# Optimization experiments

Hardware: AMD Instinct MI355X
Metric: run time of the kernel (lower is better)

The kernel has to match this reference:

```python
import jax, jax.numpy as jnp
from jax import lax
import numpy as np
from math import lgamma

N_MELS = 80; MEMORY_DIM = 512; PRENET = (256, 256)
ATTN_LSTM = 1024; ATTN_DIM = 128
N_STATIC = 8; SF = 21; N_DYN = 8; DF = 21
PRIOR_LEN = 11; ALPHA = 0.1; BETA = 0.9
DEC_LSTM = 1024; R = 2
B = 32; T_MELS = 800; T_ENC = 200


def _betabinom_pmf(k, n, a, b):
    lbeta = lambda x, y: lgamma(x) + lgamma(y) - lgamma(x + y)
    return np.exp(lgamma(n + 1) - lgamma(k + 1) - lgamma(n - k + 1) + lbeta(k + a, n - k + b) - lbeta(a, b))


def setup_inputs() -> dict:
    key = jax.random.key(0)
    ks = iter(jax.random.split(key, 40))
    w = lambda shape, s=0.05: jax.random.normal(next(ks), shape, jnp.float32) * s
    # prior filter, flipped as in the torch buffer (so cross-correlation == convolution with pmf)
    prior = np.array([_betabinom_pmf(k, PRIOR_LEN - 1, ALPHA, BETA) for k in range(PRIOR_LEN)], np.float32)[::-1].copy()
    return {
        "mels": w((B, N_MELS, T_MELS), 1.0),
        "memory": w((B, T_ENC, MEMORY_DIM), 1.0),
        "prenet_W1": w((PRENET[0], N_MELS)), "prenet_b1": jnp.zeros((PRENET[0],), jnp.float32),
        "prenet_W2": w((PRENET[1], PRENET[0])), "prenet_b2": jnp.zeros((PRENET[1],), jnp.float32),
        "attn_Wih": w((4 * ATTN_LSTM, PRENET[1] + MEMORY_DIM)), "attn_Whh": w((4 * ATTN_LSTM, ATTN_LSTM)),
        "attn_bih": jnp.zeros((4 * ATTN_LSTM,), jnp.float32), "attn_bhh": jnp.zeros((4 * ATTN_LSTM,), jnp.float32),
        "dca_Wq": w((ATTN_DIM, ATTN_LSTM)), "dca_bq": jnp.zeros((ATTN_DIM,), jnp.float32),
        "dca_V": w((N_DYN * DF, ATTN_DIM)),
        "dca_F": w((N_STATIC, 1, SF)),
        "dca_U": w((ATTN_DIM, N_STATIC)),
        "dca_T": w((ATTN_DIM, N_DYN)), "dca_Tb": jnp.zeros((ATTN_DIM,), jnp.float32),
        "dca_v": w((1, ATTN_DIM)),
        "prior": jnp.asarray(prior),
        "dec_Wih": w((4 * DEC_LSTM, ATTN_LSTM + MEMORY_DIM)), "dec_Whh": w((4 * DEC_LSTM, DEC_LSTM)),
        "dec_bih": jnp.zeros((4 * DEC_LSTM,), jnp.float32), "dec_bhh": jnp.zeros((4 * DEC_LSTM,), jnp.float32),
        "ac_W": w((N_MELS * R, DEC_LSTM + MEMORY_DIM)), "ac_b": jnp.zeros((N_MELS * R,), jnp.float32),
    }


def _lstm_cell(x, h, c, Wih, Whh, bih, bhh):
    g = x @ Wih.T + bih + h @ Whh.T + bhh
    i, f, gg, o = jnp.split(g, 4, axis=-1)  # torch gate order i,f,g,o
    c_new = jax.nn.sigmoid(f) * c + jax.nn.sigmoid(i) * jnp.tanh(gg)
    h_new = jax.nn.sigmoid(o) * jnp.tanh(c_new)
    return h_new, c_new


def _conv1d(x, k, pad, groups=1):
    # x: [B, Cin, T], k: [Cout, Cin/groups, K]; cross-correlation, like torch conv1d
    return lax.conv_general_dilated(x, k, (1,), [pad], feature_group_count=groups)


def _dca_step(query, memory, aw, prior, Wq, bq, V, Fk, U, Tw, Tb, v):
    Bsz, T = aw.shape
    # location prior: causal conv with (flipped) betabinom pmf
    p = _conv1d(aw[:, None, :], prior[None, None, :], (PRIOR_LEN - 1, 0))[:, 0, :]
    p = jnp.log(jnp.maximum(p, 1e-6))
    # dynamic filters predicted from query, applied per-batch via grouped conv
    G = jnp.tanh(query @ Wq.T + bq) @ V.T  # [B, N_DYN*DF]
    g = _conv1d(aw[None, :, :], G.reshape(Bsz * N_DYN, 1, DF), ((DF - 1) // 2, (DF - 1) // 2), groups=Bsz)
    g = g.reshape(Bsz, N_DYN, T).transpose(0, 2, 1)  # [B, T, N_DYN]
    # static location filters
    f = _conv1d(aw[:, None, :], Fk, ((SF - 1) // 2, (SF - 1) // 2)).transpose(0, 2, 1)  # [B, T, N_STATIC]
    e = (jnp.tanh(f @ U.T + g @ Tw.T + Tb) @ v.T)[:, :, 0] + p  # [B, T]
    aw_new = jax.nn.softmax(e, axis=-1)
    ctx = jnp.einsum("bt,btd->bd", aw_new, memory)
    return aw_new, ctx


def reference(mels, memory, prenet_W1, prenet_b1, prenet_W2, prenet_b2, attn_Wih, attn_Whh, attn_bih, attn_bhh, dca_Wq, dca_bq, dca_V, dca_F, dca_U, dca_T, dca_Tb, dca_v, prior, dec_Wih, dec_Whh, dec_bih, dec_bhh, ac_W, ac_b):
    Bsz, n_mels, T_mels = mels.shape
    T_enc = memory.shape[1]
    n_steps = T_mels // R
    go = jnp.zeros((Bsz, n_mels), mels.dtype)
    # teacher forcing: step t>0 consumes ground-truth frame at index t*R - 1
    tf = mels[:, :, R - 1::R][:, :, : n_steps - 1].transpose(2, 0, 1)
    frames = jnp.concatenate([go[None], tf], axis=0)  # [S, B, n_mels]
    aw0 = jnp.zeros((Bsz, T_enc), mels.dtype).at[:, 0].set(1.0)  # one-hot init attention
    carry0 = (jnp.zeros((Bsz, MEMORY_DIM), mels.dtype),
              jnp.zeros((Bsz, ATTN_LSTM), mels.dtype), jnp.zeros((Bsz, ATTN_LSTM), mels.dtype),
              jnp.zeros((Bsz, DEC_LSTM), mels.dtype), jnp.zeros((Bsz, DEC_LSTM), mels.dtype),
              aw0)

    def step(carry, frame):
        ctx, ah, acs, dh, dcs, aw = carry
        x = jax.nn.relu(frame @ prenet_W1.T + prenet_b1)
        x = jax.nn.relu(x @ prenet_W2.T + prenet_b2)
        ah, acs = _lstm_cell(jnp.concatenate([ctx, x], -1), ah, acs, attn_Wih, attn_Whh, attn_bih, attn_bhh)
        aw, ctx = _dca_step(ah, memory, aw, prior, dca_Wq, dca_bq, dca_V, dca_F, dca_U, dca_T, dca_Tb, dca_v)
        dh, dcs = _lstm_cell(jnp.concatenate([ah, ctx], -1), dh, dcs, dec_Wih, dec_Whh, dec_bih, dec_bhh)
        out = jnp.concatenate([dh, ctx], -1) @ ac_W.T + ac_b  # [B, n_mels*R]
        return (ctx, ah, acs, dh, dcs, aw), (out, aw)

    _, (outs, aws) = lax.scan(step, carry0, frames)
    # per-step [B, n_mels, R] frames concatenated along time (step-major)
    output_mels = outs.reshape(n_steps, Bsz, n_mels, R).transpose(1, 2, 0, 3).reshape(Bsz, n_mels, n_steps * R)
    alignments = aws.transpose(1, 2, 0)  # [B, T_enc, n_steps]
    return output_mels, alignments
```

## Files before the change

### kernel.cpp

```cpp
#include <hip/hip_runtime.h>
#include <hip/hip_bf16.h>

typedef unsigned short u16;
typedef unsigned int   u32;

#define NTHR 256

#define BATCH 32
#define TENC  200
#define NMELS 80
#define TMELS 800
#define NSTEP 400

#define OFF_AH    0
#define OFF_ACS   65536
#define OFF_DH    98304
#define OFF_DCS   131072
#define OFF_CTX   163840
#define OFF_AW    180224
#define OFF_FBUF  186624
#define OFF_PBUF  237824
#define OFF_GPART 244224
#define OFF_X     375296
#define FLOAT_END 3652096
#define ZERO_CNT  180224

#define B_AWIH 0
#define B_AWHH 3145728
#define B_DWIH 7340032
#define B_DWHH 13631488
#define B_ACW  17825792
#define B_WQ   18071552
#define B_MEMT 18202624

struct KArgs {
  const float *mels, *memory, *pW1, *pb1, *pW2, *pb2;
  const float *aWih, *aWhh, *abih, *abhh;
  const float *Wq, *bq, *V, *F, *U, *T, *Tb, *vv, *prior;
  const float *dWih, *dWhh, *dbih, *dbhh, *acW, *acb;
  float *out;
  float *ws;
  u16   *wb;
};

__device__ __forceinline__ float sigf(float x) {
  x = fminf(fmaxf(x, -30.f), 30.f);
  return 1.0f / (1.0f + __expf(-x));
}
__device__ __forceinline__ float ftanh(float x) {
  x = fminf(fmaxf(x, -15.f), 15.f);
  float e = __expf(2.f * x);
  return (e - 1.f) / (e + 1.f);
}
__device__ __forceinline__ float blo(u32 u) {
  union { u32 i; float f; } v; v.i = u << 16; return v.f;
}
__device__ __forceinline__ float bhi(u32 u) {
  union { u32 i; float f; } v; v.i = u & 0xffff0000u; return v.f;
}
__device__ __forceinline__ u16 f2b(float x) {
  __hip_bfloat16 h = __float2bfloat16(x);
  return *reinterpret_cast<u16*>(&h);
}

__device__ __forceinline__ void loadx(const float* src, float* xin) {
  const float4* p = (const float4*)src;
  #pragma unroll
  for (int q = 0; q < 8; ++q) {
    float4 v = p[q];
    xin[q*4+0] = v.x; xin[q*4+1] = v.y; xin[q*4+2] = v.z; xin[q*4+3] = v.w;
  }
}

__device__ __forceinline__ float dot32b(const float* xin, const u16* w) {
  const uint4* wp = (const uint4*)w;
  float acc = 0.f;
  #pragma unroll
  for (int q = 0; q < 4; ++q) {
    uint4 wv = wp[q];
    acc += blo(wv.x)*xin[q*8+0] + bhi(wv.x)*xin[q*8+1]
         + blo(wv.y)*xin[q*8+2] + bhi(wv.y)*xin[q*8+3]
         + blo(wv.z)*xin[q*8+4] + bhi(wv.z)*xin[q*8+5]
         + blo(wv.w)*xin[q*8+6] + bhi(wv.w)*xin[q*8+7];
  }
  return acc;
}

__device__ __forceinline__ float reduce8(float* smred, const float* acc) {
  const int t = threadIdx.x;
  const int b = t & 31, seg = t >> 5;
  __syncthreads();
  #pragma unroll
  for (int r = 0; r < 8; ++r) smred[(seg*8 + r)*32 + b] = acc[r];
  __syncthreads();
  const int r2 = t >> 5, b2 = t & 31;
  float tot = 0.f;
  #pragma unroll
  for (int sgi = 0; sgi < 8; ++sgi) tot += smred[(sgi*8 + r2)*32 + b2];
  return tot;
}

__device__ __forceinline__ void outproj(const KArgs& a, float* smred,
                                        const float* dh, const float* ctx,
                                        int pb, int sprev) {
  const int tid = threadIdx.x;
  const int b = tid & 31, seg = tid >> 5;
  const u16* wb = a.wb;
  float acc[8];
  #pragma unroll
  for (int r = 0; r < 8; ++r) acc[r] = 0.f;
  #pragma unroll 2
  for (int kc = 0; kc < 6; ++kc) {
    const float* src = (kc < 4) ? (dh + b*1024 + kc*256) : (ctx + b*512 + (kc-4)*256);
    float xin[32];
    loadx(src + seg*32, xin);
    #pragma unroll
    for (int r = 0; r < 8; ++r) {
      const int rr = pb*8 + r;
      acc[r] += dot32b(xin, wb + B_ACW + rr*1536 + kc*256 + seg*32);
    }
  }
  float tot = reduce8(smred, acc);
  const int r2 = tid >> 5, b2 = tid & 31;
  const int rr = pb*8 + r2;
  tot += a.acb[rr];
  a.out[(b2*NMELS + (rr >> 1))*TMELS + sprev*2 + (rr & 1)] = tot;
}

__global__ __launch_bounds__(NTHR) void init_kernel(KArgs a) {
  const int gtid = blockIdx.x*NTHR + threadIdx.x;
  const int str = gridDim.x*NTHR;
  float* ws = a.ws;
  for (int i = gtid; i < ZERO_CNT; i += str) ws[i] = 0.f;
  float* aw = ws + OFF_AW;
  for (int i = gtid; i < BATCH*TENC; i += str) aw[i] = ((i % TENC) == 0) ? 1.f : 0.f;
}

__global__ __launch_bounds__(NTHR) void conv_kernel(KArgs a) {
  const int gtid = blockIdx.x*NTHR + threadIdx.x;
  const int str = gridDim.x*NTHR;
  u16* wb = a.wb;
  for (int i = gtid; i < 3145728; i += str) wb[B_AWIH + i] = f2b(a.aWih[i]);
  for (int i = gtid; i < 4194304; i += str) wb[B_AWHH + i] = f2b(a.aWhh[i]);
  for (int i = gtid; i < 6291456; i += str) wb[B_DWIH + i] = f2b(a.dWih[i]);
  for (int i = gtid; i < 4194304; i += str) wb[B_DWHH + i] = f2b(a.dWhh[i]);
  for (int i = gtid; i < 245760;  i += str) wb[B_ACW  + i] = f2b(a.acW[i]);
  for (int i = gtid; i < 131072;  i += str) wb[B_WQ   + i] = f2b(a.Wq[i]);
  for (int i = gtid; i < 3276800; i += str) {
    const int b = i / 102400, rem = i - b*102400;
    const int d = rem / 200, t = rem - d*200;
    wb[B_MEMT + i] = f2b(a.memory[b*102400 + t*512 + d]);
  }
}

__global__ __launch_bounds__(NTHR) void prenet_kernel(KArgs a) {
  __shared__ float sm[384];
  const int tid = threadIdx.x;
  const int pair = blockIdx.x;
  const int s = pair >> 5, b = pair & 31;
  float* X = a.ws + OFF_X;
  if (tid < 80) {
    float v = 0.f;
    if (s > 0) v = a.mels[(b*NMELS + tid)*TMELS + 2*s - 1];
    sm[tid] = v;
  }
  __syncthreads();
  float a1 = a.pb1[tid];
  #pragma unroll 4
  for (int k = 0; k < 80; ++k) a1 += a.pW1[tid*80 + k] * sm[k];
  a1 = fmaxf(a1, 0.f);
  __syncthreads();
  sm[128 + tid] = a1;
  __syncthreads();
  float a2 = a.pb2[tid];
  #pragma unroll 4
  for (int k = 0; k < 256; ++k) a2 += a.pW2[tid*256 + k] * sm[128 + k];
  a2 = fmaxf(a2, 0.f);
  X[(s*BATCH + b)*256 + tid] = a2;
}

__device__ __forceinline__ void dca_step(const KArgs& a, float* sm, int b, int s,
                                         const float* ah_new, float* aw,
                                         const float* fbuf, const float* pbuf, float* ctx) {
  const int tid = threadIdx.x;
  const u16* wb = a.wb;
  float* s_ah  = sm;
  float* s_awp = sm + 1024;
  float* s_q   = sm + 1248;
  float* s_G   = sm + 1376;
  float* s_e   = sm + 1552;
  float* s_gg  = sm + 1760;
  float* s_ff  = sm + 3360;
  float* s_red = sm + 4960;
  float* s_awn = sm + 5216;
  for (int i = tid; i < 1024; i += NTHR) s_ah[i] = ah_new[b*1024 + i];
  if (tid < 220) s_awp[tid] = (tid >= 10 && tid < 210) ? aw[b*TENC + tid - 10] : 0.f;
  for (int i = tid; i < 1600; i += NTHR) s_ff[i] = fbuf[b*1600 + i];
  __syncthreads();
  {
    const int o = tid & 127, half = tid >> 7;
    const uint4* wq = (const uint4*)(wb + B_WQ + o*1024 + half*512);
    const float* xa = s_ah + half*512;
    float p = 0.f;
    #pragma unroll 8
    for (int q8 = 0; q8 < 64; ++q8) {
      uint4 w = wq[q8];
      const float* xq = xa + q8*8;
      p += blo(w.x)*xq[0] + bhi(w.x)*xq[1] + blo(w.y)*xq[2] + bhi(w.y)*xq[3]
         + blo(w.z)*xq[4] + bhi(w.z)*xq[5] + blo(w.w)*xq[6] + bhi(w.w)*xq[7];
    }
    s_red[tid] = p;
  }
  __syncthreads();
  if (tid < 128) s_q[tid] = ftanh(s_red[tid] + s_red[128 + tid] + a.bq[tid]);
  __syncthreads();
  if (tid < 168) {
    const float4* vp = (const float4*)(a.V + tid*128);
    float p = 0.f;
    #pragma unroll
    for (int q4 = 0; q4 < 32; ++q4) {
      float4 w = vp[q4];
      const float* xq = s_q + q4*4;
      p += w.x*xq[0] + w.y*xq[1] + w.z*xq[2] + w.w*xq[3];
    }
    s_G[tid] = p;
  }
  __syncthreads();
  for (int idx = tid; idx < 1600; idx += NTHR) {
    const int pos = idx >> 3, d = idx & 7;
    float p = 0.f;
    #pragma unroll
    for (int tau = 0; tau < 21; ++tau) p += s_awp[pos + tau] * s_G[d*21 + tau];
    s_gg[idx] = p;
  }
  __syncthreads();
  #pragma unroll 1
  for (int ro = 0; ro < 4; ++ro) {
    const int pos = ro*64 + (tid >> 2), sub = tid & 3;
    float av = 0.f;
    if (pos < 200) {
      const float* fpos = s_ff + pos*8;
      const float* gpos = s_gg + pos*8;
      #pragma unroll 4
      for (int fi = 0; fi < 32; ++fi) {
        const int ff = sub*32 + fi;
        const float4* Up = (const float4*)(a.U + ff*8);
        const float4* Tp = (const float4*)(a.T + ff*8);
        float4 u0 = Up[0], u1 = Up[1], t0 = Tp[0], t1 = Tp[1];
        float h = a.Tb[ff];
        h += u0.x*fpos[0] + u0.y*fpos[1] + u0.z*fpos[2] + u0.w*fpos[3]
           + u1.x*fpos[4] + u1.y*fpos[5] + u1.z*fpos[6] + u1.w*fpos[7];
        h += t0.x*gpos[0] + t0.y*gpos[1] + t0.z*gpos[2] + t0.w*gpos[3]
           + t1.x*gpos[4] + t1.y*gpos[5] + t1.z*gpos[6] + t1.w*gpos[7];
        av += a.vv[ff] * ftanh(h);
      }
    }
    av += __shfl_xor(av, 1);
    av += __shfl_xor(av, 2);
    if (sub == 0 && pos < 200) s_e[pos] = av + pbuf[b*TENC + pos];
  }
  __syncthreads();
  float mval = (tid < 200) ? s_e[tid] : -1e30f;
  #pragma unroll
  for (int off = 32; off > 0; off >>= 1) mval = fmaxf(mval, __shfl_xor(mval, off));
  if ((tid & 63) == 0) s_red[tid >> 6] = mval;
  __syncthreads();
  const float m = fmaxf(fmaxf(s_red[0], s_red[1]), fmaxf(s_red[2], s_red[3]));
  const float ex = (tid < 200) ? __expf(s_e[tid] - m) : 0.f;
  float sv = ex;
  #pragma unroll
  for (int off = 32; off > 0; off >>= 1) sv += __shfl_xor(sv, off);
  if ((tid & 63) == 0) s_red[4 + (tid >> 6)] = sv;
  __syncthreads();
  const float inv = 1.f / (s_red[4] + s_red[5] + s_red[6] + s_red[7]);
  if (tid < 200) {
    const float awv = ex * inv;
    aw[b*TENC + tid] = awv;
    s_awn[tid] = awv;
    a.out[2048000 + b*80000 + tid*400 + s] = awv;
  }
  __syncthreads();
  #pragma unroll 1
  for (int d = tid; d < 512; d += NTHR) {
    const uint4* mp = (const uint4*)(wb + B_MEMT + b*102400 + d*200);
    float p = 0.f;
    #pragma unroll 5
    for (int q = 0; q < 25; ++q) {
      uint4 v = mp[q];
      const float* aa = s_awn + q*8;
      p += blo(v.x)*aa[0] + bhi(v.x)*aa[1] + blo(v.y)*aa[2] + bhi(v.y)*aa[3]
         + blo(v.z)*aa[4] + bhi(v.z)*aa[5] + blo(v.w)*aa[6] + bhi(v.w)*aa[7];
    }
    ctx[b*512 + d] = p;
  }
}

__global__ __launch_bounds__(NTHR) void p1_kernel(KArgs a, int s) {
  __shared__ float sm[2560];
  float* smred = sm;
  float* smg   = sm + 2048;
  const int tid = threadIdx.x;
  const int bid = blockIdx.x;
  float* ws = a.ws;
  const u16* wb = a.wb;
  float* ah_prev = ws + OFF_AH + ((s & 1) ? 32768 : 0);
  float* ah_new  = ws + OFF_AH + ((s & 1) ? 0 : 32768);
  float* acs = ws + OFF_ACS;
  float* dh  = ws + OFF_DH;
  float* ctx = ws + OFF_CTX;
  float* aw  = ws + OFF_AW;
  float* fbuf  = ws + OFF_FBUF;
  float* pbuf  = ws + OFF_PBUF;
  float* gpart = ws + OFF_GPART;
  float* X     = ws + OFF_X;

  if (bid < 512) {
    const int b = tid & 31, seg = tid >> 5, u0 = bid*2;
    const float* Xs = X + s*BATCH*256;
    float acc[8];
    #pragma unroll
    for (int r = 0; r < 8; ++r) acc[r] = 0.f;
    #pragma unroll 2
    for (int kc = 0; kc < 7; ++kc) {
      const float* src = (kc < 2)  ? (ctx + b*512 + kc*256)
                       : (kc == 2) ? (Xs + b*256)
                                   : (ah_prev + b*1024 + (kc-3)*256);
      float xin[32];
      loadx(src + seg*32, xin);
      #pragma unroll
      for (int r = 0; r < 8; ++r) {
        const int rr = (r>>1)*1024 + u0 + (r&1);
        const u16* wr = (kc < 3) ? (wb + B_AWIH + rr*768 + kc*256 + seg*32)
                                 : (wb + B_AWHH + rr*1024 + (kc-3)*256 + seg*32);
        acc[r] += dot32b(xin, wr);
      }
    }
    float tot = reduce8(smred, acc);
    {
      const int r2 = tid >> 5, b2 = tid & 31;
      const int rr = (r2>>1)*1024 + u0 + (r2&1);
      smg[r2*32 + b2] = tot + a.abih[rr] + a.abhh[rr];
    }
    __syncthreads();
    if (tid < 64) {
      const int u = tid >> 5, b2 = tid & 31;
      const int j = u0 + u;
      const float gi = smg[(0+u)*32+b2], gf = smg[(2+u)*32+b2];
      const float gg = smg[(4+u)*32+b2], go = smg[(6+u)*32+b2];
      const float c = sigf(gf)*acs[b2*1024+j] + sigf(gi)*ftanh(gg);
      acs[b2*1024+j] = c;
      ah_new[b2*1024+j] = sigf(go)*ftanh(c);
    }
  } else if (bid < 1024) {
    const int b = tid & 31, seg = tid >> 5, j2 = bid - 512;
    float acc[8];
    #pragma unroll
    for (int r = 0; r < 8; ++r) acc[r] = 0.f;
    #pragma unroll 2
    for (int kc = 0; kc < 4; ++kc) {
      float xin[32];
      loadx(dh + b*1024 + kc*256 + seg*32, xin);
      #pragma unroll
      for (int r = 0; r < 8; ++r) {
        const int rr = j2*8 + r;
        acc[r] += dot32b(xin, wb + B_DWHH + rr*1024 + kc*256 + seg*32);
      }
    }
    float tot = reduce8(smred, acc);
    const int r2 = tid >> 5, b2 = tid & 31;
    const int rr = j2*8 + r2;
    gpart[rr*32 + b2] = tot + a.dbih[rr] + a.dbhh[rr];
  } else if (bid < 1044) {
    if (s > 0) outproj(a, smred, dh, ctx, bid - 1024, s - 1);
  } else {
    const int b4 = bid - 1044;
    if (tid < 224) sm[tid] = (tid >= 10 && tid < 210) ? aw[b4*TENC + tid - 10] : 0.f;
    __syncthreads();
    if (tid < 200) {
      #pragma unroll
      for (int j = 0; j < 8; ++j) {
        float p = 0.f;
        #pragma unroll
        for (int tau = 0; tau < 21; ++tau) p += sm[tid + tau] * a.F[j*21 + tau];
        fbuf[(b4*TENC + tid)*8 + j] = p;
      }
      float pp = 0.f;
      #pragma unroll
      for (int tau = 0; tau < 11; ++tau) pp += sm[tid + tau] * a.prior[tau];
      pbuf[b4*TENC + tid] = __logf(fmaxf(pp, 1e-6f));
    }
  }
}

__global__ __launch_bounds__(NTHR) void p2_kernel(KArgs a, int s) {
  __shared__ float sm[5536];
  const int tid = threadIdx.x;
  const int bid = blockIdx.x;
  float* ws = a.ws;
  const u16* wb = a.wb;
  float* ah_new = ws + OFF_AH + ((s & 1) ? 0 : 32768);
  float* ctx = ws + OFF_CTX;
  float* aw  = ws + OFF_AW;
  float* fbuf  = ws + OFF_FBUF;
  float* pbuf  = ws + OFF_PBUF;
  float* gpart = ws + OFF_GPART;

  if (bid < 32) {
    dca_step(a, sm, bid, s, ah_new, aw, fbuf, pbuf, ctx);
  } else {
    const int b = tid & 31, seg = tid >> 5, job = bid - 32;
    float acc[8];
    #pragma unroll
    for (int r = 0; r < 8; ++r) acc[r] = 0.f;
    #pragma unroll 2
    for (int kc = 0; kc < 4; ++kc) {
      float xin[32];
      loadx(ah_new + b*1024 + kc*256 + seg*32, xin);
      #pragma unroll
      for (int r = 0; r < 8; ++r) {
        const int rr = job*8 + r;
        acc[r] += dot32b(xin, wb + B_DWIH + rr*1536 + kc*256 + seg*32);
      }
    }
    float tot = reduce8(sm, acc);
    const int r2 = tid >> 5, b2 = tid & 31;
    const int rr = job*8 + r2;
    gpart[rr*32 + b2] += tot;
  }
}

__global__ __launch_bounds__(NTHR) void p3_kernel(KArgs a, int s) {
  __shared__ float sm[2560];
  float* smred = sm;
  float* smg   = sm + 2048;
  const int tid = threadIdx.x;
  const int bid = blockIdx.x;
  float* ws = a.ws;
  const u16* wb = a.wb;
  float* dh  = ws + OFF_DH;
  float* dcs = ws + OFF_DCS;
  float* ctx = ws + OFF_CTX;
  float* gpart = ws + OFF_GPART;

  const int b = tid & 31, seg = tid >> 5, u0 = bid*2;
  float acc[8];
  #pragma unroll
  for (int r = 0; r < 8; ++r) acc[r] = 0.f;
  #pragma unroll 2
  for (int kc = 0; kc < 2; ++kc) {
    float xin[32];
    loadx(ctx + b*512 + kc*256 + seg*32, xin);
    #pragma unroll
    for (int r = 0; r < 8; ++r) {
      const int rr = (r>>1)*1024 + u0 + (r&1);
      acc[r] += dot32b(xin, wb + B_DWIH + rr*1536 + 1024 + kc*256 + seg*32);
    }
  }
  float tot = reduce8(smred, acc);
  {
    const int r2 = tid >> 5, b2 = tid & 31;
    const int rr = (r2>>1)*1024 + u0 + (r2&1);
    smg[r2*32 + b2] = tot + gpart[rr*32 + b2];
  }
  __syncthreads();
  if (tid < 64) {
    const int u = tid >> 5, b2 = tid & 31;
    const int j = u0 + u;
    const float gi = smg[(0+u)*32+b2], gf = smg[(2+u)*32+b2];
    const float gg = smg[(4+u)*32+b2], go = smg[(6+u)*32+b2];
    const float c = sigf(gf)*dcs[b2*1024+j] + sigf(gi)*ftanh(gg);
    dcs[b2*1024+j] = c;
    dh[b2*1024+j] = sigf(go)*ftanh(c);
  }
}

__global__ __launch_bounds__(NTHR) void ep_kernel(KArgs a) {
  __shared__ float sm[2048];
  float* ws = a.ws;
  outproj(a, sm, ws + OFF_DH, ws + OFF_CTX, blockIdx.x, NSTEP - 1);
}

extern "C" void kernel_launch(void* const* d_in, const int* in_sizes, int n_in,
                              void* d_out, int out_size, void* d_ws, size_t ws_size,
                              hipStream_t stream) {
  (void)in_sizes; (void)n_in; (void)out_size; (void)ws_size;
  KArgs a;
  a.mels   = (const float*)d_in[0];
  a.memory = (const float*)d_in[1];
  a.pW1 = (const float*)d_in[2];  a.pb1 = (const float*)d_in[3];
  a.pW2 = (const float*)d_in[4];  a.pb2 = (const float*)d_in[5];
  a.aWih = (const float*)d_in[6]; a.aWhh = (const float*)d_in[7];
  a.abih = (const float*)d_in[8]; a.abhh = (const float*)d_in[9];
  a.Wq = (const float*)d_in[10];  a.bq = (const float*)d_in[11];
  a.V  = (const float*)d_in[12];  a.F  = (const float*)d_in[13];
  a.U  = (const float*)d_in[14];  a.T  = (const float*)d_in[15];
  a.Tb = (const float*)d_in[16];  a.vv = (const float*)d_in[17];
  a.prior = (const float*)d_in[18];
  a.dWih = (const float*)d_in[19]; a.dWhh = (const float*)d_in[20];
  a.dbih = (const float*)d_in[21]; a.dbhh = (const float*)d_in[22];
  a.acW  = (const float*)d_in[23]; a.acb  = (const float*)d_in[24];
  a.out = (float*)d_out;
  a.ws  = (float*)((char*)d_ws + 256);
  a.wb  = (u16*)(a.ws + FLOAT_END);

  hipLaunchKernelGGL(init_kernel, dim3(512), dim3(NTHR), 0, stream, a);
  hipLaunchKernelGGL(conv_kernel, dim3(2048), dim3(NTHR), 0, stream, a);
  hipLaunchKernelGGL(prenet_kernel, dim3(NSTEP*BATCH), dim3(NTHR), 0, stream, a);
  for (int s = 0; s < NSTEP; ++s) {
    hipLaunchKernelGGL(p1_kernel, dim3(1076), dim3(NTHR), 0, stream, a, s);
    hipLaunchKernelGGL(p2_kernel, dim3(544), dim3(NTHR), 0, stream, a, s);
    hipLaunchKernelGGL(p3_kernel, dim3(512), dim3(NTHR), 0, stream, a, s);
  }
  hipLaunchKernelGGL(ep_kernel, dim3(20), dim3(NTHR), 0, stream, a);
}
```

Baseline: 61.56 ms.

## Fuse per-step decoder kernels into one persistent kernel with grid barriers

```diff
diff --git a/kernel.cpp b/kernel.cpp
--- a/kernel.cpp
+++ b/kernel.cpp
@@ -4,6 +4,7 @@
 typedef unsigned short u16;
 typedef unsigned int   u32;
 
+#define NBLK 512
 #define NTHR 256
 
 #define BATCH 32
@@ -16,14 +17,16 @@
 #define OFF_ACS   65536
 #define OFF_DH    98304
 #define OFF_DCS   131072
-#define OFF_CTX   163840
-#define OFF_AW    180224
-#define OFF_FBUF  186624
-#define OFF_PBUF  237824
-#define OFF_GPART 244224
-#define OFF_X     375296
-#define FLOAT_END 3652096
-#define ZERO_CNT  180224
+#define OFF_CTX0  163840
+#define OFF_CTX1  180224
+#define OFF_AW    196608
+#define OFF_FBUF  203008
+#define OFF_PBUF  254208
+#define OFF_GPA   260608
+#define OFF_GPB   391680
+#define OFF_X     522752
+#define FLOAT_END 3799552
+#define ZERO_CNT  196608
 
 #define B_AWIH 0
 #define B_AWHH 3145728
@@ -41,6 +44,7 @@
   float *out;
   float *ws;
   u16   *wb;
+  u32   *bar;
 };
 
 __device__ __forceinline__ float sigf(float x) {
@@ -61,6 +65,20 @@
 __device__ __forceinline__ u16 f2b(float x) {
   __hip_bfloat16 h = __float2bfloat16(x);
   return *reinterpret_cast<u16*>(&h);
+}
+
+__device__ __forceinline__ void gbar(u32* bar, unsigned* epoch) {
+  __syncthreads();
+  if (threadIdx.x == 0) {
+    __threadfence();
+    *epoch += NBLK;
+    __hip_atomic_fetch_add(bar, 1u, __ATOMIC_RELAXED, __HIP_MEMORY_SCOPE_AGENT);
+    while (__hip_atomic_load(bar, __ATOMIC_RELAXED, __HIP_MEMORY_SCOPE_AGENT) < *epoch) {
+      __builtin_amdgcn_s_sleep(2);
+    }
+    __threadfence();
+  }
+  __syncthreads();
 }
 
 __device__ __forceinline__ void loadx(const float* src, float* xin) {
@@ -100,11 +118,139 @@
   return tot;
 }
 
+
+__device__ __forceinline__ void j1job(const KArgs& a, float* smred, float* smg,
+                                      int u0, int s, const float* ctxp,
+                                      const float* ah_prev, float* ah_new,
+                                      float* acs, const float* X) {
+  const int tid = threadIdx.x, b = tid & 31, seg = tid >> 5;
+  const u16* wb = a.wb;
+  const float* Xs = X + s*BATCH*256;
+  float acc[8];
+  #pragma unroll
+  for (int r = 0; r < 8; ++r) acc[r] = 0.f;
+  #pragma unroll 2
+  for (int kc = 0; kc < 7; ++kc) {
+    const float* src = (kc < 2)  ? (ctxp + b*512 + kc*256)
+                     : (kc == 2) ? (Xs + b*256)
+                                 : (ah_prev + b*1024 + (kc-3)*256);
+    float xin[32];
+    loadx(src + seg*32, xin);
+    #pragma unroll
+    for (int r = 0; r < 8; ++r) {
+      const int rr = (r>>1)*1024 + u0 + (r&1);
+      const u16* wr = (kc < 3) ? (wb + B_AWIH + rr*768 + kc*256 + seg*32)
+                               : (wb + B_AWHH + rr*1024 + (kc-3)*256 + seg*32);
+      acc[r] += dot32b(xin, wr);
+    }
+  }
+  float tot = reduce8(smred, acc);
+  {
+    const int r2 = tid >> 5, b2 = tid & 31;
+    const int rr = (r2>>1)*1024 + u0 + (r2&1);
+    smg[r2*32 + b2] = tot + a.abih[rr] + a.abhh[rr];
+  }
+  __syncthreads();
+  if (tid < 64) {
+    const int u = tid >> 5, b2 = tid & 31;
+    const int j = u0 + u;
+    const float gi = smg[(0+u)*32+b2], gf = smg[(2+u)*32+b2];
+    const float gg = smg[(4+u)*32+b2], go = smg[(6+u)*32+b2];
+    const float c = sigf(gf)*acs[b2*1024+j] + sigf(gi)*ftanh(gg);
+    acs[b2*1024+j] = c;
+    ah_new[b2*1024+j] = sigf(go)*ftanh(c);
+  }
+  __syncthreads();
+}
+
+__device__ __forceinline__ void p3job(const KArgs& a, float* smred, float* smg,
+                                      int u0, const float* ctxc,
+                                      float* dh, float* dcs,
+                                      const float* gpa, const float* gpb) {
+  const int tid = threadIdx.x, b = tid & 31, seg = tid >> 5;
+  const u16* wb = a.wb;
+  float acc[8];
+  #pragma unroll
+  for (int r = 0; r < 8; ++r) acc[r] = 0.f;
+  #pragma unroll 2
+  for (int kc = 0; kc < 2; ++kc) {
+    float xin[32];
+    loadx(ctxc + b*512 + kc*256 + seg*32, xin);
+    #pragma unroll
+    for (int r = 0; r < 8; ++r) {
+      const int rr = (r>>1)*1024 + u0 + (r&1);
+      acc[r] += dot32b(xin, wb + B_DWIH + rr*1536 + 1024 + kc*256 + seg*32);
+    }
+  }
+  float tot = reduce8(smred, acc);
+  {
+    const int r2 = tid >> 5, b2 = tid & 31;
+    const int rr = (r2>>1)*1024 + u0 + (r2&1);
+    smg[r2*32 + b2] = tot + gpa[rr*32 + b2] + gpb[rr*32 + b2];
+  }
+  __syncthreads();
+  if (tid < 64) {
+    const int u = tid >> 5, b2 = tid & 31;
+    const int j = u0 + u;
+    const float gi = smg[(0+u)*32+b2], gf = smg[(2+u)*32+b2];
+    const float gg = smg[(4+u)*32+b2], go = smg[(6+u)*32+b2];
+    const float c = sigf(gf)*dcs[b2*1024+j] + sigf(gi)*ftanh(gg);
+    dcs[b2*1024+j] = c;
+    dh[b2*1024+j] = sigf(go)*ftanh(c);
+  }
+  __syncthreads();
+}
+
+__device__ __forceinline__ void j2job(const KArgs& a, float* smred, int j2,
+                                      const float* dh, float* gpa) {
+  const int tid = threadIdx.x, b = tid & 31, seg = tid >> 5;
+  const u16* wb = a.wb;
+  float acc[8];
+  #pragma unroll
+  for (int r = 0; r < 8; ++r) acc[r] = 0.f;
+  #pragma unroll 2
+  for (int kc = 0; kc < 4; ++kc) {
+    float xin[32];
+    loadx(dh + b*1024 + kc*256 + seg*32, xin);
+    #pragma unroll
+    for (int r = 0; r < 8; ++r) {
+      const int rr = j2*8 + r;
+      acc[r] += dot32b(xin, wb + B_DWHH + rr*1024 + kc*256 + seg*32);
+    }
+  }
+  float tot = reduce8(smred, acc);
+  const int r2 = tid >> 5, b2 = tid & 31;
+  const int rr = j2*8 + r2;
+  gpa[rr*32 + b2] = tot + a.dbih[rr] + a.dbhh[rr];
+}
+
+__device__ __forceinline__ void dwihjob(const KArgs& a, float* smred, int job,
+                                        const float* ah_new, float* gpb) {
+  const int tid = threadIdx.x, b = tid & 31, seg = tid >> 5;
+  const u16* wb = a.wb;
+  float acc[8];
+  #pragma unroll
+  for (int r = 0; r < 8; ++r) acc[r] = 0.f;
+  #pragma unroll 2
+  for (int kc = 0; kc < 4; ++kc) {
+    float xin[32];
+    loadx(ah_new + b*1024 + kc*256 + seg*32, xin);
+    #pragma unroll
+    for (int r = 0; r < 8; ++r) {
+      const int rr = job*8 + r;
+      acc[r] += dot32b(xin, wb + B_DWIH + rr*1536 + kc*256 + seg*32);
+    }
+  }
+  float tot = reduce8(smred, acc);
+  const int r2 = tid >> 5, b2 = tid & 31;
+  const int rr = job*8 + r2;
+  gpb[rr*32 + b2] = tot;
+}
+
 __device__ __forceinline__ void outproj(const KArgs& a, float* smred,
                                         const float* dh, const float* ctx,
                                         int pb, int sprev) {
-  const int tid = threadIdx.x;
-  const int b = tid & 31, seg = tid >> 5;
+  const int tid = threadIdx.x, b = tid & 31, seg = tid >> 5;
   const u16* wb = a.wb;
   float acc[8];
   #pragma unroll
@@ -127,56 +273,25 @@
   a.out[(b2*NMELS + (rr >> 1))*TMELS + sprev*2 + (rr & 1)] = tot;
 }
 
-__global__ __launch_bounds__(NTHR) void init_kernel(KArgs a) {
-  const int gtid = blockIdx.x*NTHR + threadIdx.x;
-  const int str = gridDim.x*NTHR;
-  float* ws = a.ws;
-  for (int i = gtid; i < ZERO_CNT; i += str) ws[i] = 0.f;
-  float* aw = ws + OFF_AW;
-  for (int i = gtid; i < BATCH*TENC; i += str) aw[i] = ((i % TENC) == 0) ? 1.f : 0.f;
-}
-
-__global__ __launch_bounds__(NTHR) void conv_kernel(KArgs a) {
-  const int gtid = blockIdx.x*NTHR + threadIdx.x;
-  const int str = gridDim.x*NTHR;
-  u16* wb = a.wb;
-  for (int i = gtid; i < 3145728; i += str) wb[B_AWIH + i] = f2b(a.aWih[i]);
-  for (int i = gtid; i < 4194304; i += str) wb[B_AWHH + i] = f2b(a.aWhh[i]);
-  for (int i = gtid; i < 6291456; i += str) wb[B_DWIH + i] = f2b(a.dWih[i]);
-  for (int i = gtid; i < 4194304; i += str) wb[B_DWHH + i] = f2b(a.dWhh[i]);
-  for (int i = gtid; i < 245760;  i += str) wb[B_ACW  + i] = f2b(a.acW[i]);
-  for (int i = gtid; i < 131072;  i += str) wb[B_WQ   + i] = f2b(a.Wq[i]);
-  for (int i = gtid; i < 3276800; i += str) {
-    const int b = i / 102400, rem = i - b*102400;
-    const int d = rem / 200, t = rem - d*200;
-    wb[B_MEMT + i] = f2b(a.memory[b*102400 + t*512 + d]);
-  }
-}
-
-__global__ __launch_bounds__(NTHR) void prenet_kernel(KArgs a) {
-  __shared__ float sm[384];
+__device__ __forceinline__ void j4job(const KArgs& a, float* sm, int b4,
+                                      const float* aw, float* fbuf, float* pbuf) {
   const int tid = threadIdx.x;
-  const int pair = blockIdx.x;
-  const int s = pair >> 5, b = pair & 31;
-  float* X = a.ws + OFF_X;
-  if (tid < 80) {
-    float v = 0.f;
-    if (s > 0) v = a.mels[(b*NMELS + tid)*TMELS + 2*s - 1];
-    sm[tid] = v;
-  }
-  __syncthreads();
-  float a1 = a.pb1[tid];
-  #pragma unroll 4
-  for (int k = 0; k < 80; ++k) a1 += a.pW1[tid*80 + k] * sm[k];
-  a1 = fmaxf(a1, 0.f);
-  __syncthreads();
-  sm[128 + tid] = a1;
-  __syncthreads();
-  float a2 = a.pb2[tid];
-  #pragma unroll 4
-  for (int k = 0; k < 256; ++k) a2 += a.pW2[tid*256 + k] * sm[128 + k];
-  a2 = fmaxf(a2, 0.f);
-  X[(s*BATCH + b)*256 + tid] = a2;
+  if (tid < 224) sm[tid] = (tid >= 10 && tid < 210) ? aw[b4*TENC + tid - 10] : 0.f;
+  __syncthreads();
+  if (tid < 200) {
+    #pragma unroll
+    for (int j = 0; j < 8; ++j) {
+      float p = 0.f;
+      #pragma unroll
+      for (int tau = 0; tau < 21; ++tau) p += sm[tid + tau] * a.F[j*21 + tau];
+      fbuf[(b4*TENC + tid)*8 + j] = p;
+    }
+    float pp = 0.f;
+    #pragma unroll
+    for (int tau = 0; tau < 11; ++tau) pp += sm[tid + tau] * a.prior[tau];
+    pbuf[b4*TENC + tid] = __logf(fmaxf(pp, 1e-6f));
+  }
+  __syncthreads();
 }
 
 __device__ __forceinline__ void dca_step(const KArgs& a, float* sm, int b, int s,
@@ -193,6 +308,7 @@
   float* s_ff  = sm + 3360;
   float* s_red = sm + 4960;
   float* s_awn = sm + 5216;
+  __syncthreads();
   for (int i = tid; i < 1024; i += NTHR) s_ah[i] = ah_new[b*1024 + i];
   if (tid < 220) s_awp[tid] = (tid >= 10 && tid < 210) ? aw[b*TENC + tid - 10] : 0.f;
   for (int i = tid; i < 1600; i += NTHR) s_ff[i] = fbuf[b*1600 + i];
@@ -293,191 +409,115 @@
     }
     ctx[b*512 + d] = p;
   }
-}
-
-__global__ __launch_bounds__(NTHR) void p1_kernel(KArgs a, int s) {
-  __shared__ float sm[2560];
+  __syncthreads();
+}
+
+__global__ void init_bar(KArgs a) {
+  if (threadIdx.x == 0) *a.bar = 0u;
+}
+
+__global__ __launch_bounds__(NTHR) void init_kernel(KArgs a) {
+  const int gtid = blockIdx.x*NTHR + threadIdx.x;
+  const int str = gridDim.x*NTHR;
+  float* ws = a.ws;
+  for (int i = gtid; i < ZERO_CNT; i += str) ws[i] = 0.f;
+  float* aw = ws + OFF_AW;
+  for (int i = gtid; i < BATCH*TENC; i += str) aw[i] = ((i % TENC) == 0) ? 1.f : 0.f;
+}
+
+__global__ __launch_bounds__(NTHR) void conv_kernel(KArgs a) {
+  const int gtid = blockIdx.x*NTHR + threadIdx.x;
+  const int str = gridDim.x*NTHR;
+  u16* wb = a.wb;
+  for (int i = gtid; i < 3145728; i += str) wb[B_AWIH + i] = f2b(a.aWih[i]);
+  for (int i = gtid; i < 4194304; i += str) wb[B_AWHH + i] = f2b(a.aWhh[i]);
+  for (int i = gtid; i < 6291456; i += str) wb[B_DWIH + i] = f2b(a.dWih[i]);
+  for (int i = gtid; i < 4194304; i += str) wb[B_DWHH + i] = f2b(a.dWhh[i]);
+  for (int i = gtid; i < 245760;  i += str) wb[B_ACW  + i] = f2b(a.acW[i]);
+  for (int i = gtid; i < 131072;  i += str) wb[B_WQ   + i] = f2b(a.Wq[i]);
+  for (int i = gtid; i < 3276800; i += str) {
+    const int b = i / 102400, rem = i - b*102400;
+    const int d = rem / 200, t = rem - d*200;
+    wb[B_MEMT + i] = f2b(a.memory[b*102400 + t*512 + d]);
+  }
+}
+
+__global__ __launch_bounds__(NTHR) void prenet_kernel(KArgs a) {
+  __shared__ float sm[384];
+  const int tid = threadIdx.x;
+  const int pair = blockIdx.x;
+  const int s = pair >> 5, b = pair & 31;
+  float* X = a.ws + OFF_X;
+  if (tid < 80) {
+    float v = 0.f;
+    if (s > 0) v = a.mels[(b*NMELS + tid)*TMELS + 2*s - 1];
+    sm[tid] = v;
+  }
+  __syncthreads();
+  float a1 = a.pb1[tid];
+  #pragma unroll 4
+  for (int k = 0; k < 80; ++k) a1 += a.pW1[tid*80 + k] * sm[k];
+  a1 = fmaxf(a1, 0.f);
+  __syncthreads();
+  sm[128 + tid] = a1;
+  __syncthreads();
+  float a2 = a.pb2[tid];
+  #pragma unroll 4
+  for (int k = 0; k < 256; ++k) a2 += a.pW2[tid*256 + k] * sm[128 + k];
+  a2 = fmaxf(a2, 0.f);
+  X[(s*BATCH + b)*256 + tid] = a2;
+}
+
+__global__ __launch_bounds__(NTHR, 2) void decoder_kernel(KArgs a) {
+  __shared__ float sm[5536];
   float* smred = sm;
   float* smg   = sm + 2048;
-  const int tid = threadIdx.x;
   const int bid = blockIdx.x;
   float* ws = a.ws;
-  const u16* wb = a.wb;
-  float* ah_prev = ws + OFF_AH + ((s & 1) ? 32768 : 0);
-  float* ah_new  = ws + OFF_AH + ((s & 1) ? 0 : 32768);
   float* acs = ws + OFF_ACS;
   float* dh  = ws + OFF_DH;
-  float* ctx = ws + OFF_CTX;
+  float* dcs = ws + OFF_DCS;
   float* aw  = ws + OFF_AW;
   float* fbuf  = ws + OFF_FBUF;
   float* pbuf  = ws + OFF_PBUF;
-  float* gpart = ws + OFF_GPART;
+  float* gpa   = ws + OFF_GPA;
+  float* gpb   = ws + OFF_GPB;
   float* X     = ws + OFF_X;
-
-  if (bid < 512) {
-    const int b = tid & 31, seg = tid >> 5, u0 = bid*2;
-    const float* Xs = X + s*BATCH*256;
-    float acc[8];
-    #pragma unroll
-    for (int r = 0; r < 8; ++r) acc[r] = 0.f;
-    #pragma unroll 2
-    for (int kc = 0; kc < 7; ++kc) {
-      const float* src = (kc < 2)  ? (ctx + b*512 + kc*256)
-                       : (kc == 2) ? (Xs + b*256)
-                                   : (ah_prev + b*1024 + (kc-3)*256);
-      float xin[32];
-      loadx(src + seg*32, xin);
-      #pragma unroll
-      for (int r = 0; r < 8; ++r) {
-        const int rr = (r>>1)*1024 + u0 + (r&1);
-        const u16* wr = (kc < 3) ? (wb + B_AWIH + rr*768 + kc*256 + seg*32)
-                                 : (wb + B_AWHH + rr*1024 + (kc-3)*256 + seg*32);
-        acc[r] += dot32b(xin, wr);
+  unsigned epoch = 0;
+
+  for (int s = 0; s < NSTEP; ++s) {
+    float* ah_prev = ws + OFF_AH + ((s & 1) ? 0 : 32768);
+    float* ah_new  = ws + OFF_AH + ((s & 1) ? 32768 : 0);
+    float* ctxc = ws + ((s & 1) ? OFF_CTX1 : OFF_CTX0);
+    float* ctxp = ws + ((s & 1) ? OFF_CTX0 : OFF_CTX1);
+
+    if (s > 0) p3job(a, smred, smg, bid*2, ctxp, dh, dcs, gpa, gpb);
+    j1job(a, smred, smg, bid*2, s, ctxp, ah_prev, ah_new, acs, X);
+    if (bid >= 480) j4job(a, sm, bid - 480, aw, fbuf, pbuf);
+    gbar(a.bar, &epoch);
+
+    if (bid >= 480) {
+      dca_step(a, sm, bid - 480, s, ah_new, aw, fbuf, pbuf, ctxc);
+    } else {
+      dwihjob(a, smred, bid, ah_new, gpb);
+      const int j1i = bid + 480;
+      if (j1i < 512) dwihjob(a, smred, j1i, ah_new, gpb);
+      else           j2job(a, smred, j1i - 512, dh, gpa);
+      if (bid < 84) {
+        const int j2i = bid + 960;
+        if (j2i < 1024)   j2job(a, smred, j2i - 512, dh, gpa);
+        else if (s > 0)   outproj(a, smred, dh, ctxp, j2i - 1024, s - 1);
       }
     }
-    float tot = reduce8(smred, acc);
-    {
-      const int r2 = tid >> 5, b2 = tid & 31;
-      const int rr = (r2>>1)*1024 + u0 + (r2&1);
-      smg[r2*32 + b2] = tot + a.abih[rr] + a.abhh[rr];
-    }
-    __syncthreads();
-    if (tid < 64) {
-      const int u = tid >> 5, b2 = tid & 31;
-      const int j = u0 + u;
-      const float gi = smg[(0+u)*32+b2], gf = smg[(2+u)*32+b2];
-      const float gg = smg[(4+u)*32+b2], go = smg[(6+u)*32+b2];
-      const float c = sigf(gf)*acs[b2*1024+j] + sigf(gi)*ftanh(gg);
-      acs[b2*1024+j] = c;
-      ah_new[b2*1024+j] = sigf(go)*ftanh(c);
-    }
-  } else if (bid < 1024) {
-    const int b = tid & 31, seg = tid >> 5, j2 = bid - 512;
-    float acc[8];
-    #pragma unroll
-    for (int r = 0; r < 8; ++r) acc[r] = 0.f;
-    #pragma unroll 2
-    for (int kc = 0; kc < 4; ++kc) {
-      float xin[32];
-      loadx(dh + b*1024 + kc*256 + seg*32, xin);
-      #pragma unroll
-      for (int r = 0; r < 8; ++r) {
-        const int rr = j2*8 + r;
-        acc[r] += dot32b(xin, wb + B_DWHH + rr*1024 + kc*256 + seg*32);
-      }
-    }
-    float tot = reduce8(smred, acc);
-    const int r2 = tid >> 5, b2 = tid & 31;
-    const int rr = j2*8 + r2;
-    gpart[rr*32 + b2] = tot + a.dbih[rr] + a.dbhh[rr];
-  } else if (bid < 1044) {
-    if (s > 0) outproj(a, smred, dh, ctx, bid - 1024, s - 1);
-  } else {
-    const int b4 = bid - 1044;
-    if (tid < 224) sm[tid] = (tid >= 10 && tid < 210) ? aw[b4*TENC + tid - 10] : 0.f;
-    __syncthreads();
-    if (tid < 200) {
-      #pragma unroll
-      for (int j = 0; j < 8; ++j) {
-        float p = 0.f;
-        #pragma unroll
-        for (int tau = 0; tau < 21; ++tau) p += sm[tid + tau] * a.F[j*21 + tau];
-        fbuf[(b4*TENC + tid)*8 + j] = p;
-      }
-      float pp = 0.f;
-      #pragma unroll
-      for (int tau = 0; tau < 11; ++tau) pp += sm[tid + tau] * a.prior[tau];
-      pbuf[b4*TENC + tid] = __logf(fmaxf(pp, 1e-6f));
-    }
-  }
-}
-
-__global__ __launch_bounds__(NTHR) void p2_kernel(KArgs a, int s) {
-  __shared__ float sm[5536];
-  const int tid = threadIdx.x;
-  const int bid = blockIdx.x;
-  float* ws = a.ws;
-  const u16* wb = a.wb;
-  float* ah_new = ws + OFF_AH + ((s & 1) ? 0 : 32768);
-  float* ctx = ws + OFF_CTX;
-  float* aw  = ws + OFF_AW;
-  float* fbuf  = ws + OFF_FBUF;
-  float* pbuf  = ws + OFF_PBUF;
-  float* gpart = ws + OFF_GPART;
-
-  if (bid < 32) {
-    dca_step(a, sm, bid, s, ah_new, aw, fbuf, pbuf, ctx);
-  } else {
-    const int b = tid & 31, seg = tid >> 5, job = bid - 32;
-    float acc[8];
-    #pragma unroll
-    for (int r = 0; r < 8; ++r) acc[r] = 0.f;
-    #pragma unroll 2
-    for (int kc = 0; kc < 4; ++kc) {
-      float xin[32];
-      loadx(ah_new + b*1024 + kc*256 + seg*32, xin);
-      #pragma unroll
-      for (int r = 0; r < 8; ++r) {
-        const int rr = job*8 + r;
-        acc[r] += dot32b(xin, wb + B_DWIH + rr*1536 + kc*256 + seg*32);
-      }
-    }
-    float tot = reduce8(sm, acc);
-    const int r2 = tid >> 5, b2 = tid & 31;
-    const int rr = job*8 + r2;
-    gpart[rr*32 + b2] += tot;
-  }
-}
-
-__global__ __launch_bounds__(NTHR) void p3_kernel(KArgs a, int s) {
-  __shared__ float sm[2560];
-  float* smred = sm;
-  float* smg   = sm + 2048;
-  const int tid = threadIdx.x;
-  const int bid = blockIdx.x;
-  float* ws = a.ws;
-  const u16* wb = a.wb;
-  float* dh  = ws + OFF_DH;
-  float* dcs = ws + OFF_DCS;
-  float* ctx = ws + OFF_CTX;
-  float* gpart = ws + OFF_GPART;
-
-  const int b = tid & 31, seg = tid >> 5, u0 = bid*2;
-  float acc[8];
-  #pragma unroll
-  for (int r = 0; r < 8; ++r) acc[r] = 0.f;
-  #pragma unroll 2
-  for (int kc = 0; kc < 2; ++kc) {
-    float xin[32];
-    loadx(ctx + b*512 + kc*256 + seg*32, xin);
-    #pragma unroll
-    for (int r = 0; r < 8; ++r) {
-      const int rr = (r>>1)*1024 + u0 + (r&1);
-      acc[r] += dot32b(xin, wb + B_DWIH + rr*1536 + 1024 + kc*256 + seg*32);
-    }
-  }
-  float tot = reduce8(smred, acc);
+    gbar(a.bar, &epoch);
+  }
+
   {
-    const int r2 = tid >> 5, b2 = tid & 31;
-    const int rr = (r2>>1)*1024 + u0 + (r2&1);
-    smg[r2*32 + b2] = tot + gpart[rr*32 + b2];
-  }
-  __syncthreads();
-  if (tid < 64) {
-    const int u = tid >> 5, b2 = tid & 31;
-    const int j = u0 + u;
-    const float gi = smg[(0+u)*32+b2], gf = smg[(2+u)*32+b2];
-    const float gg = smg[(4+u)*32+b2], go = smg[(6+u)*32+b2];
-    const float c = sigf(gf)*dcs[b2*1024+j] + sigf(gi)*ftanh(gg);
-    dcs[b2*1024+j] = c;
-    dh[b2*1024+j] = sigf(go)*ftanh(c);
-  }
-}
-
-__global__ __launch_bounds__(NTHR) void ep_kernel(KArgs a) {
-  __shared__ float sm[2048];
-  float* ws = a.ws;
-  outproj(a, sm, ws + OFF_DH, ws + OFF_CTX, blockIdx.x, NSTEP - 1);
+    float* ctx399 = ws + OFF_CTX1;
+    p3job(a, smred, smg, bid*2, ctx399, dh, dcs, gpa, gpb);
+    gbar(a.bar, &epoch);
+    if (bid < 20) outproj(a, smred, dh, ctx399, bid, NSTEP - 1);
+  }
 }
 
 extern "C" void kernel_launch(void* const* d_in, const int* in_sizes, int n_in,
@@ -500,16 +540,13 @@
   a.dbih = (const float*)d_in[21]; a.dbhh = (const float*)d_in[22];
   a.acW  = (const float*)d_in[23]; a.acb  = (const float*)d_in[24];
   a.out = (float*)d_out;
+  a.bar = (u32*)d_ws;
   a.ws  = (float*)((char*)d_ws + 256);
   a.wb  = (u16*)(a.ws + FLOAT_END);
 
+  hipLaunchKernelGGL(init_bar, dim3(1), dim3(64), 0, stream, a);
   hipLaunchKernelGGL(init_kernel, dim3(512), dim3(NTHR), 0, stream, a);
   hipLaunchKernelGGL(conv_kernel, dim3(2048), dim3(NTHR), 0, stream, a);
   hipLaunchKernelGGL(prenet_kernel, dim3(NSTEP*BATCH), dim3(NTHR), 0, stream, a);
-  for (int s = 0; s < NSTEP; ++s) {
-    hipLaunchKernelGGL(p1_kernel, dim3(1076), dim3(NTHR), 0, stream, a, s);
-    hipLaunchKernelGGL(p2_kernel, dim3(544), dim3(NTHR), 0, stream, a, s);
-    hipLaunchKernelGGL(p3_kernel, dim3(512), dim3(NTHR), 0, stream, a, s);
-  }
-  hipLaunchKernelGGL(ep_kernel, dim3(20), dim3(NTHR), 0, stream, a);
-}
+  hipLaunchKernelGGL(decoder_kernel, dim3(NBLK), dim3(NTHR), 0, stream, a);
+}
```

New measurement: 113.4 ms. 84.1% more time.
